# Optimization experiments

Hardware: AMD Instinct MI355X
Metric: run time of the kernel (lower is better)

The kernel has to match this reference:

```python
import jax, jax.numpy as jnp
import numpy as np

B, C, H, W = 4, 64, 128, 128
CO, K, PAD, STRIDE = 64, 3, 1, 1


def setup_inputs() -> dict:
    key = jax.random.key(0)
    k1, k2, k3 = jax.random.split(key, 3)
    x = jax.random.normal(k1, (B, C, H, W), dtype=jnp.float32)
    # small offset weights so predicted offsets stay near the regular grid
    w_off = jax.random.normal(k2, (2 * K * K, C, K, K), dtype=jnp.float32) * 0.01
    b_off = jnp.zeros((2 * K * K,), dtype=jnp.float32)
    w_def = jax.random.normal(k3, (CO, C, K, K), dtype=jnp.float32) * (1.0 / np.sqrt(C * K * K))
    return {"x": x, "w_off": w_off, "b_off": b_off, "w_def": w_def}


def _deform_forward(x, w_off, b_off, w_def):
    Bs, Cs, Hs, Ws = x.shape
    Co = w_def.shape[0]
    KK = K * K
    # offset conv: [B, 2*K*K, Ho, Wo]
    off = jax.lax.conv_general_dilated(
        x, w_off, (STRIDE, STRIDE), [(PAD, PAD), (PAD, PAD)],
        dimension_numbers=("NCHW", "OIHW", "NCHW"))
    off = off + b_off[None, :, None, None]
    Ho, Wo = off.shape[2], off.shape[3]
    off = off.reshape(Bs, KK, 2, Ho, Wo)  # channel 2k -> dy, 2k+1 -> dx
    ky = (jnp.arange(KK) // K).astype(x.dtype)
    kx = (jnp.arange(KK) % K).astype(x.dtype)
    gy = (jnp.arange(Ho) * STRIDE - PAD).astype(x.dtype)
    gx = (jnp.arange(Wo) * STRIDE - PAD).astype(x.dtype)
    # sampling positions per (batch, tap, out_y, out_x)
    py = off[:, :, 0] + ky[None, :, None, None] + gy[None, None, :, None]
    px = off[:, :, 1] + kx[None, :, None, None] + gx[None, None, None, :]
    y0 = jnp.floor(py)
    x0 = jnp.floor(px)
    dy = py - y0
    dx = px - x0
    y0i = y0.astype(jnp.int32)
    x0i = x0.astype(jnp.int32)
    xf = x.reshape(Bs, Cs, Hs * Ws)

    def gather(iy, ix):
        valid = (iy >= 0) & (iy < Hs) & (ix >= 0) & (ix < Ws)
        idx = jnp.clip(iy, 0, Hs - 1) * Ws + jnp.clip(ix, 0, Ws - 1)  # [B,KK,Ho,Wo]
        g = jax.vmap(lambda xb, ib: jnp.take(xb, ib.reshape(-1), axis=1))(xf, idx)
        g = g.reshape(Bs, Cs, KK, Ho, Wo)
        return g * valid[:, None].astype(x.dtype)

    # bilinear sample with zero padding outside the image (torchvision semantics)
    sampled = gather(y0i, x0i) * ((1 - dy) * (1 - dx))[:, None]
    sampled = sampled + gather(y0i, x0i + 1) * ((1 - dy) * dx)[:, None]
    sampled = sampled + gather(y0i + 1, x0i) * (dy * (1 - dx))[:, None]
    sampled = sampled + gather(y0i + 1, x0i + 1) * (dy * dx)[:, None]
    # conv-style weighted accumulation over (channel, tap)
    return jnp.einsum("bckhw,ock->bohw", sampled, w_def.reshape(Co, Cs, KK))


def reference(x, w_off, b_off, w_def):
    return _deform_forward(x, w_off, b_off, w_def)
```

## Files before the change

kernel.cpp:

```cpp
#include <hip/hip_runtime.h>
#include <math.h>


typedef short  v4s __attribute__((ext_vector_type(4)));
typedef short  v8s __attribute__((ext_vector_type(8)));
typedef float  v4f __attribute__((ext_vector_type(4)));
typedef float  v2f __attribute__((ext_vector_type(2)));

namespace {
constexpr int Bn = 4, Cn = 64, Hn = 128, Wn = 128, COn = 64;
constexpr int HWn = 16384;
constexpr int CKn = 576;
constexpr int TILE = 16;
constexpr int RS = 580;
constexpr int HW2 = 132;
constexpr int XPITCH = HW2 * 16;
constexpr size_t XH_OFF   = 0;
constexpr size_t ASWZ_OFF = 2230272;
constexpr size_t AOFF_OFF = ASWZ_OFF + 18432;
}

__device__ __forceinline__ unsigned short f2bf(float f) {
    union { float f; unsigned int u; } v; v.f = f;
    unsigned int u = v.u;
    u += 0x7fffu + ((u >> 16) & 1u);
    return (unsigned short)(u >> 16);
}
__device__ __forceinline__ unsigned int pack2bf(float a, float b) {
    return (unsigned int)f2bf(a) | ((unsigned int)f2bf(b) << 16);
}
__device__ __forceinline__ v2f unpk(unsigned int u) {
    v2f r;
    r.x = __uint_as_float(u << 16);
    r.y = __uint_as_float(u & 0xffff0000u);
    return r;
}

__global__ __launch_bounds__(256) void k_halo(const float* __restrict__ x,
                                              unsigned int* __restrict__ xh) {
    __shared__ float tile[64][65];
    const int tid  = threadIdx.x;
    const int lane = tid & 63;
    const int grp  = tid >> 6;
    const int b    = blockIdx.x >> 8;
    const int hw0  = (blockIdx.x & 255) << 6;
#pragma unroll
    for (int r = 0; r < 16; ++r) {
        const int c = (r << 2) + grp;
        tile[c][lane] = x[(b * Cn + c) * HWn + hw0 + lane];
    }
    __syncthreads();
    const int h = lane >> 5;
    const int m = lane & 31;
#pragma unroll
    for (int r = 0; r < 8; ++r) {
        const int hwl = (r << 3) + (grp << 1) + h;
        const int hw  = hw0 + hwl;
        const int yy  = hw >> 7;
        const int xx  = hw & (Wn - 1);
        const unsigned int u = pack2bf(tile[2 * m][hwl], tile[2 * m + 1][hwl]);
        xh[((size_t)(b * HW2 + yy + 2) * HW2 + (xx + 2)) * 32 + m] = u;
    }
}

__global__ __launch_bounds__(256) void k_prep(const float* __restrict__ w_def,
                                              const float* __restrict__ w_off,
                                              unsigned short* __restrict__ aswz,
                                              unsigned short* __restrict__ aoff) {
    const int idx = blockIdx.x * 256 + threadIdx.x;
    if (idx < 36864) {
        const int j = idx & 7;
        const int l = (idx >> 3) & 63;
        const int s = (idx >> 9) % 18;
        const int r = idx / 9216;
        const int co = 16 * r + (l & 15);
        const int kk = 32 * s + 4 * (l >> 4) + (j & 3) + 16 * (j >> 2);
        const int tap = kk >> 6, c = kk & 63;
        aswz[idx] = f2bf(w_def[co * CKn + c * 9 + tap]);
    } else {
        const int i2 = idx - 36864;
        const int j = i2 & 7;
        const int l = (i2 >> 3) & 63;
        const int s = (i2 >> 9) % 18;
        const int r = i2 / 9216;
        const int co = 16 * r + (l & 15);
        const int kk = 32 * s + 4 * (l >> 4) + (j & 3) + 16 * (j >> 2);
        const int tap = kk >> 6, c = kk & 63;
        aoff[i2] = (co < 18) ? f2bf(w_off[co * CKn + c * 9 + tap]) : (unsigned short)0;
    }
}

__global__ __launch_bounds__(256, 6) void k_deform(const uint2* __restrict__ xh2,
                                                   const unsigned short* __restrict__ aoff,
                                                   const float* __restrict__ b_off,
                                                   const unsigned short* __restrict__ aswz,
                                                   float* __restrict__ out) {
    __shared__ unsigned short Bl[TILE * RS];
    __shared__ float part[4][18][16];
    __shared__ float offl[18][16];
    uint2* Bl2 = (uint2*)Bl;
    const int tid  = threadIdx.x;
    const int lane = tid & 63;
    const int wid  = tid >> 6;
    const int g    = lane >> 4;
    const int c15  = lane & 15;
    const int q    = lane & 15;
    const int pq   = lane >> 4;
    const int b    = blockIdx.x >> 10;
    const int p0   = (blockIdx.x & 1023) * TILE;
    const int pix  = (wid << 2) + pq;
    const int p    = p0 + pix;
    const int oy   = p >> 7;
    const int ox   = p & (Wn - 1);
    const int xbase = b * (HW2 * HW2 * 16);

#pragma unroll
    for (int k = 0; k < 9; ++k) {
        const int sy = oy + k / 3 - 1;
        const int sx = ox + k % 3 - 1;
        const uint2 t = xh2[xbase + ((sy + 2) * HW2 + (sx + 2)) * 16 + q];
        Bl2[pix * 145 + k * 16 + q] = t;
    }
    __syncthreads();

    {
        v4f pa00 = {0.f,0.f,0.f,0.f};
        v4f pa10 = {0.f,0.f,0.f,0.f};
        for (int s = wid; s < 18; s += 4) {
            const int kb = 32 * s + 4 * g;
            const unsigned short* b0p = &Bl[c15 * RS + kb];
            const v4s lo0 = *reinterpret_cast<const v4s*>(b0p);
            const v4s hi0 = *reinterpret_cast<const v4s*>(b0p + 16);
            const v8s bb0 = {lo0[0],lo0[1],lo0[2],lo0[3],hi0[0],hi0[1],hi0[2],hi0[3]};
            const v8s a0 = *reinterpret_cast<const v8s*>(aoff + (size_t)(0 * 18 + s) * 512 + lane * 8);
            const v8s a1 = *reinterpret_cast<const v8s*>(aoff + (size_t)(1 * 18 + s) * 512 + lane * 8);
            pa00 = __builtin_amdgcn_mfma_f32_16x16x32_bf16(a0, bb0, pa00, 0, 0, 0);
            pa10 = __builtin_amdgcn_mfma_f32_16x16x32_bf16(a1, bb0, pa10, 0, 0, 0);
        }
#pragma unroll
        for (int r = 0; r < 4; ++r) {
            const int co0 = (g << 2) + r;
            part[wid][co0][c15] = pa00[r];
            const int co1 = 16 + (g << 2) + r;
            if (co1 < 18)
                part[wid][co1][c15] = pa10[r];
        }
    }
    __syncthreads();
    for (int idx = tid; idx < 288; idx += 256) {
        const int ch = idx >> 4, px = idx & 15;
        offl[ch][px] = part[0][ch][px] + part[1][ch][px] + part[2][ch][px]
                     + part[3][ch][px] + b_off[ch];
    }
    __syncthreads();

#pragma unroll
    for (int k = 0; k < 9; ++k) {
        const float py = offl[2 * k][pix]     + (float)(oy + k / 3 - 1);
        const float px = offl[2 * k + 1][pix] + (float)(ox + k % 3 - 1);
        const float fy = floorf(py);
        const float fx = floorf(px);
        const float ay = py - fy;
        const float ax = px - fx;
        int iy0 = (int)fy;
        int ix0 = (int)fx;
        iy0 = max(-2, min(iy0, 128));
        ix0 = max(-2, min(ix0, 128));
        const float w00 = (1.f - ay) * (1.f - ax);
        const float w01 = (1.f - ay) * ax;
        const float w10 = ay * (1.f - ax);
        const float w11 = ay * ax;
        const uint2* r0 = xh2 + xbase + ((iy0 + 2) * HW2 + (ix0 + 2)) * 16 + q;
        const uint2 u00 = r0[0];
        const uint2 u01 = r0[16];
        const uint2 u10 = r0[XPITCH];
        const uint2 u11 = r0[XPITCH + 16];
        v2f va = unpk(u00.x) * w00;
        va += unpk(u01.x) * w01;
        va += unpk(u10.x) * w10;
        va += unpk(u11.x) * w11;
        v2f vb = unpk(u00.y) * w00;
        vb += unpk(u01.y) * w01;
        vb += unpk(u10.y) * w10;
        vb += unpk(u11.y) * w11;
        Bl2[pix * 145 + k * 16 + q] = make_uint2(pack2bf(va.x, va.y), pack2bf(vb.x, vb.y));
    }
    __syncthreads();

    v4f acc0 = {0.f,0.f,0.f,0.f};
    const unsigned short* arow = aswz + (size_t)wid * 9216 + lane * 8;
#pragma unroll
    for (int s = 0; s < 18; ++s) {
        const v8s a = *reinterpret_cast<const v8s*>(arow + s * 512);
        const int kb = 32 * s + 4 * g;
        const unsigned short* b0p = &Bl[c15 * RS + kb];
        const v4s lo0 = *reinterpret_cast<const v4s*>(b0p);
        const v4s hi0 = *reinterpret_cast<const v4s*>(b0p + 16);
        const v8s bb0 = {lo0[0],lo0[1],lo0[2],lo0[3],hi0[0],hi0[1],hi0[2],hi0[3]};
        acc0 = __builtin_amdgcn_mfma_f32_16x16x32_bf16(a, bb0, acc0, 0, 0, 0);
    }
    const int co = (wid << 4) + (g << 2);
    float* op = out + ((size_t)(b * COn + co)) * HWn + p0 + c15;
#pragma unroll
    for (int r = 0; r < 4; ++r)
        op[(size_t)r * HWn] = acc0[r];
}

extern "C" void kernel_launch(void* const* d_in, const int* in_sizes, int n_in,
                              void* d_out, int out_size, void* d_ws, size_t ws_size,
                              hipStream_t stream) {
    const float* x     = (const float*)d_in[0];
    const float* w_off = (const float*)d_in[1];
    const float* b_off = (const float*)d_in[2];
    const float* w_def = (const float*)d_in[3];
    float* outp = (float*)d_out;
    float* wsf  = (float*)d_ws;
    unsigned int* xh = (unsigned int*)(wsf + XH_OFF);
    unsigned short* aswz = (unsigned short*)(wsf + ASWZ_OFF);
    unsigned short* aoff = (unsigned short*)(wsf + AOFF_OFF);

    hipMemsetAsync(xh, 0, (size_t)Bn * HW2 * HW2 * Cn * 2, stream);
    k_halo<<<Bn * 256, 256, 0, stream>>>(x, xh);
    k_prep<<<216, 256, 0, stream>>>(w_def, w_off, aswz, aoff);
    k_deform<<<Bn * (HWn / TILE), 256, 0, stream>>>((const uint2*)xh, aoff, b_off, aswz, outp);
}
```

Before: 56.21 us.

## Merge prep kernels with border-only zeroing and split offset conv into own kernel

The halo-transpose and weight-swizzle kernels become one launch, and the full-buffer memset is replaced by blocks that zero only the two-pixel border of the padded input. The deform kernel is split in two: an offset-conv kernel writes the offsets to global memory, and a main kernel reads them back to do the bilinear sampling and the MFMA accumulation. This removes a memset pass and launch overhead and lowers per-kernel LDS and register pressure. In exchange it adds a kernel launch, a global round trip for the offsets, and a second staging of the input tile.

New measurement: 54.73 us. 2.6% less time.

```diff
diff --git a/kernel.cpp b/kernel.cpp
--- a/kernel.cpp
+++ b/kernel.cpp
@@ -18,6 +18,7 @@
 constexpr size_t XH_OFF   = 0;
 constexpr size_t ASWZ_OFF = 2230272;
 constexpr size_t AOFF_OFF = ASWZ_OFF + 18432;
+constexpr size_t OFFG_OFF = AOFF_OFF + 9216;
 }
 
 __device__ __forceinline__ unsigned short f2bf(float f) {
@@ -36,68 +37,88 @@
     return r;
 }
 
-__global__ __launch_bounds__(256) void k_halo(const float* __restrict__ x,
-                                              unsigned int* __restrict__ xh) {
-    __shared__ float tile[64][65];
-    const int tid  = threadIdx.x;
-    const int lane = tid & 63;
-    const int grp  = tid >> 6;
-    const int b    = blockIdx.x >> 8;
-    const int hw0  = (blockIdx.x & 255) << 6;
-#pragma unroll
-    for (int r = 0; r < 16; ++r) {
-        const int c = (r << 2) + grp;
-        tile[c][lane] = x[(b * Cn + c) * HWn + hw0 + lane];
-    }
-    __syncthreads();
-    const int h = lane >> 5;
-    const int m = lane & 31;
-#pragma unroll
-    for (int r = 0; r < 8; ++r) {
-        const int hwl = (r << 3) + (grp << 1) + h;
-        const int hw  = hw0 + hwl;
-        const int yy  = hw >> 7;
-        const int xx  = hw & (Wn - 1);
-        const unsigned int u = pack2bf(tile[2 * m][hwl], tile[2 * m + 1][hwl]);
-        xh[((size_t)(b * HW2 + yy + 2) * HW2 + (xx + 2)) * 32 + m] = u;
-    }
-}
-
-__global__ __launch_bounds__(256) void k_prep(const float* __restrict__ w_def,
-                                              const float* __restrict__ w_off,
-                                              unsigned short* __restrict__ aswz,
-                                              unsigned short* __restrict__ aoff) {
-    const int idx = blockIdx.x * 256 + threadIdx.x;
-    if (idx < 36864) {
-        const int j = idx & 7;
-        const int l = (idx >> 3) & 63;
-        const int s = (idx >> 9) % 18;
-        const int r = idx / 9216;
-        const int co = 16 * r + (l & 15);
-        const int kk = 32 * s + 4 * (l >> 4) + (j & 3) + 16 * (j >> 2);
-        const int tap = kk >> 6, c = kk & 63;
-        aswz[idx] = f2bf(w_def[co * CKn + c * 9 + tap]);
+__global__ __launch_bounds__(256) void k_pre(const float* __restrict__ x,
+                                             const float* __restrict__ w_def,
+                                             const float* __restrict__ w_off,
+                                             unsigned int* __restrict__ xh,
+                                             unsigned short* __restrict__ aswz,
+                                             unsigned short* __restrict__ aoff) {
+    const int blk = blockIdx.x;
+    const int tid = threadIdx.x;
+    if (blk < 1024) {
+        __shared__ float tile[64][65];
+        const int lane = tid & 63;
+        const int grp  = tid >> 6;
+        const int b    = blk >> 8;
+        const int hw0  = (blk & 255) << 6;
+#pragma unroll
+        for (int r = 0; r < 16; ++r) {
+            const int c = (r << 2) + grp;
+            tile[c][lane] = x[(b * Cn + c) * HWn + hw0 + lane];
+        }
+        __syncthreads();
+        const int h = lane >> 5;
+        const int m = lane & 31;
+#pragma unroll
+        for (int r = 0; r < 8; ++r) {
+            const int hwl = (r << 3) + (grp << 1) + h;
+            const int hw  = hw0 + hwl;
+            const int yy  = hw >> 7;
+            const int xx  = hw & (Wn - 1);
+            const unsigned int u = pack2bf(tile[2 * m][hwl], tile[2 * m + 1][hwl]);
+            xh[((size_t)(b * HW2 + yy + 2) * HW2 + (xx + 2)) * 32 + m] = u;
+        }
+    } else if (blk < 1240) {
+        const int idx = (blk - 1024) * 256 + tid;
+        if (idx < 36864) {
+            const int j = idx & 7;
+            const int l = (idx >> 3) & 63;
+            const int s = (idx >> 9) % 18;
+            const int r = idx / 9216;
+            const int co = 16 * r + (l & 15);
+            const int kk = 32 * s + 4 * (l >> 4) + (j & 3) + 16 * (j >> 2);
+            const int tap = kk >> 6, c = kk & 63;
+            aswz[idx] = f2bf(w_def[co * CKn + c * 9 + tap]);
+        } else {
+            const int i2 = idx - 36864;
+            const int j = i2 & 7;
+            const int l = (i2 >> 3) & 63;
+            const int s = (i2 >> 9) % 18;
+            const int r = i2 / 9216;
+            const int co = 16 * r + (l & 15);
+            const int kk = 32 * s + 4 * (l >> 4) + (j & 3) + 16 * (j >> 2);
+            const int tap = kk >> 6, c = kk & 63;
+            aoff[i2] = (co < 18) ? f2bf(w_off[co * CKn + c * 9 + tap]) : (unsigned short)0;
+        }
     } else {
-        const int i2 = idx - 36864;
-        const int j = i2 & 7;
-        const int l = (i2 >> 3) & 63;
-        const int s = (i2 >> 9) % 18;
-        const int r = i2 / 9216;
-        const int co = 16 * r + (l & 15);
-        const int kk = 32 * s + 4 * (l >> 4) + (j & 3) + 16 * (j >> 2);
-        const int tap = kk >> 6, c = kk & 63;
-        aoff[i2] = (co < 18) ? f2bf(w_off[co * CKn + c * 9 + tap]) : (unsigned short)0;
-    }
-}
-
-__global__ __launch_bounds__(256, 6) void k_deform(const uint2* __restrict__ xh2,
+        const int i = (blk - 1240) * 256 + tid;
+        const int b = i / 16640;
+        const int r = i % 16640;
+        int yy, xx, q;
+        if (r < 8448) {
+            const int y = r / 2112;
+            yy = (y < 2) ? y : 128 + y;
+            const int rem = r % 2112;
+            xx = rem >> 4;
+            q  = rem & 15;
+        } else {
+            const int r2 = r - 8448;
+            yy = 2 + (r2 >> 6);
+            const int rem = r2 & 63;
+            const int xs = rem >> 4;
+            xx = (xs < 2) ? xs : 128 + xs;
+            q  = rem & 15;
+        }
+        ((uint2*)xh)[(((size_t)b * HW2 + yy) * HW2 + xx) * 16 + q] = make_uint2(0u, 0u);
+    }
+}
+
+__global__ __launch_bounds__(256, 4) void k_offset(const uint2* __restrict__ xh2,
                                                    const unsigned short* __restrict__ aoff,
                                                    const float* __restrict__ b_off,
-                                                   const unsigned short* __restrict__ aswz,
-                                                   float* __restrict__ out) {
+                                                   float* __restrict__ off_g) {
     __shared__ unsigned short Bl[TILE * RS];
     __shared__ float part[4][18][16];
-    __shared__ float offl[18][16];
     uint2* Bl2 = (uint2*)Bl;
     const int tid  = threadIdx.x;
     const int lane = tid & 63;
@@ -118,46 +139,69 @@
     for (int k = 0; k < 9; ++k) {
         const int sy = oy + k / 3 - 1;
         const int sx = ox + k % 3 - 1;
-        const uint2 t = xh2[xbase + ((sy + 2) * HW2 + (sx + 2)) * 16 + q];
-        Bl2[pix * 145 + k * 16 + q] = t;
-    }
-    __syncthreads();
-
-    {
-        v4f pa00 = {0.f,0.f,0.f,0.f};
-        v4f pa10 = {0.f,0.f,0.f,0.f};
-        for (int s = wid; s < 18; s += 4) {
-            const int kb = 32 * s + 4 * g;
-            const unsigned short* b0p = &Bl[c15 * RS + kb];
-            const v4s lo0 = *reinterpret_cast<const v4s*>(b0p);
-            const v4s hi0 = *reinterpret_cast<const v4s*>(b0p + 16);
-            const v8s bb0 = {lo0[0],lo0[1],lo0[2],lo0[3],hi0[0],hi0[1],hi0[2],hi0[3]};
-            const v8s a0 = *reinterpret_cast<const v8s*>(aoff + (size_t)(0 * 18 + s) * 512 + lane * 8);
-            const v8s a1 = *reinterpret_cast<const v8s*>(aoff + (size_t)(1 * 18 + s) * 512 + lane * 8);
-            pa00 = __builtin_amdgcn_mfma_f32_16x16x32_bf16(a0, bb0, pa00, 0, 0, 0);
-            pa10 = __builtin_amdgcn_mfma_f32_16x16x32_bf16(a1, bb0, pa10, 0, 0, 0);
-        }
-#pragma unroll
-        for (int r = 0; r < 4; ++r) {
-            const int co0 = (g << 2) + r;
-            part[wid][co0][c15] = pa00[r];
-            const int co1 = 16 + (g << 2) + r;
-            if (co1 < 18)
-                part[wid][co1][c15] = pa10[r];
-        }
+        Bl2[pix * 145 + k * 16 + q] = xh2[xbase + ((sy + 2) * HW2 + (sx + 2)) * 16 + q];
+    }
+    __syncthreads();
+
+    v4f pa0 = {0.f,0.f,0.f,0.f};
+    v4f pa1 = {0.f,0.f,0.f,0.f};
+    for (int s = wid; s < 18; s += 4) {
+        const int kb = 32 * s + 4 * g;
+        const unsigned short* b0p = &Bl[c15 * RS + kb];
+        const v4s lo0 = *reinterpret_cast<const v4s*>(b0p);
+        const v4s hi0 = *reinterpret_cast<const v4s*>(b0p + 16);
+        const v8s bb0 = {lo0[0],lo0[1],lo0[2],lo0[3],hi0[0],hi0[1],hi0[2],hi0[3]};
+        const v8s a0 = *reinterpret_cast<const v8s*>(aoff + (size_t)(0 * 18 + s) * 512 + lane * 8);
+        const v8s a1 = *reinterpret_cast<const v8s*>(aoff + (size_t)(1 * 18 + s) * 512 + lane * 8);
+        pa0 = __builtin_amdgcn_mfma_f32_16x16x32_bf16(a0, bb0, pa0, 0, 0, 0);
+        pa1 = __builtin_amdgcn_mfma_f32_16x16x32_bf16(a1, bb0, pa1, 0, 0, 0);
+    }
+#pragma unroll
+    for (int r = 0; r < 4; ++r) {
+        const int co0 = (g << 2) + r;
+        part[wid][co0][c15] = pa0[r];
+        const int co1 = 16 + (g << 2) + r;
+        if (co1 < 18)
+            part[wid][co1][c15] = pa1[r];
     }
     __syncthreads();
     for (int idx = tid; idx < 288; idx += 256) {
-        const int ch = idx >> 4, px = idx & 15;
-        offl[ch][px] = part[0][ch][px] + part[1][ch][px] + part[2][ch][px]
-                     + part[3][ch][px] + b_off[ch];
-    }
+        const int px = idx / 18, ch = idx % 18;
+        off_g[((size_t)(b * HWn + p0)) * 18 + idx] =
+            part[0][ch][px] + part[1][ch][px] + part[2][ch][px] + part[3][ch][px] + b_off[ch];
+    }
+}
+
+__global__ __launch_bounds__(256, 4) void k_main(const uint2* __restrict__ xh2,
+                                                 const float* __restrict__ off_g,
+                                                 const unsigned short* __restrict__ aswz,
+                                                 float* __restrict__ out) {
+    __shared__ unsigned short Bl[TILE * RS];
+    __shared__ float offl[16][18];
+    uint2* Bl2 = (uint2*)Bl;
+    const int tid  = threadIdx.x;
+    const int lane = tid & 63;
+    const int wid  = tid >> 6;
+    const int g    = lane >> 4;
+    const int c15  = lane & 15;
+    const int q    = lane & 15;
+    const int pq   = lane >> 4;
+    const int b    = blockIdx.x >> 10;
+    const int p0   = (blockIdx.x & 1023) * TILE;
+    const int pix  = (wid << 2) + pq;
+    const int p    = p0 + pix;
+    const int oy   = p >> 7;
+    const int ox   = p & (Wn - 1);
+    const int xbase = b * (HW2 * HW2 * 16);
+
+    for (int idx = tid; idx < 288; idx += 256)
+        offl[idx / 18][idx % 18] = off_g[((size_t)(b * HWn + p0)) * 18 + idx];
     __syncthreads();
 
 #pragma unroll
     for (int k = 0; k < 9; ++k) {
-        const float py = offl[2 * k][pix]     + (float)(oy + k / 3 - 1);
-        const float px = offl[2 * k + 1][pix] + (float)(ox + k % 3 - 1);
+        const float py = offl[pix][2 * k]     + (float)(oy + k / 3 - 1);
+        const float px = offl[pix][2 * k + 1] + (float)(ox + k % 3 - 1);
         const float fy = floorf(py);
         const float fx = floorf(px);
         const float ay = py - fy;
@@ -218,9 +262,9 @@
     unsigned int* xh = (unsigned int*)(wsf + XH_OFF);
     unsigned short* aswz = (unsigned short*)(wsf + ASWZ_OFF);
     unsigned short* aoff = (unsigned short*)(wsf + AOFF_OFF);
-
-    hipMemsetAsync(xh, 0, (size_t)Bn * HW2 * HW2 * Cn * 2, stream);
-    k_halo<<<Bn * 256, 256, 0, stream>>>(x, xh);
-    k_prep<<<216, 256, 0, stream>>>(w_def, w_off, aswz, aoff);
-    k_deform<<<Bn * (HWn / TILE), 256, 0, stream>>>((const uint2*)xh, aoff, b_off, aswz, outp);
-}
+    float* off_g = wsf + OFFG_OFF;
+
+    k_pre<<<1500, 256, 0, stream>>>(x, w_def, w_off, xh, aswz, aoff);
+    k_offset<<<Bn * (HWn / TILE), 256, 0, stream>>>((const uint2*)xh, aoff, b_off, off_g);
+    k_main<<<Bn * (HWn / TILE), 256, 0, stream>>>((const uint2*)xh, off_g, aswz, outp);
+}
```
